# Kernel tuning notes

Hardware: AMD Instinct MI355X
Metric: run time of the kernel (lower is better)

The kernel has to match this reference:

```python
import jax, jax.numpy as jnp
import numpy as np

NX, NY, NZ = 432, 496, 1
C = 64
B = 4
P = 64000


def setup_inputs() -> dict:
    key = jax.random.key(0)
    k1, k2, k3 = jax.random.split(key, 3)
    pillar_features = jax.random.normal(k1, (P, C), dtype=jnp.float32)
    # Build unique (batch, y, x) cells so the scatter has no duplicate targets
    # (torch advanced-index assignment with duplicates is order-dependent).
    n_cells = B * NY * NX
    flat = jax.random.permutation(k2, n_cells)[:P]  # unique global cell ids
    b = flat // (NY * NX)
    rem = flat % (NY * NX)
    y = rem // NX
    x = rem % NX
    z = jnp.zeros_like(b)
    voxel_coords = jnp.stack([b, z, y, x], axis=1).astype(jnp.int32)  # [P, 4]
    return {
        "pillar_features": pillar_features,
        "voxel_coords": voxel_coords,
        "batch_size": B,
    }


def reference(pillar_features, voxel_coords, batch_size):
    # Global scatter: one fused pass instead of the per-batch Python loop.
    coords = voxel_coords.astype(jnp.int32)
    # per-sample spatial index, exactly as in the torch code: z + y*nx + x
    spatial_idx = coords[:, 1] + coords[:, 2] * NX + coords[:, 3]
    global_idx = coords[:, 0] * (NY * NX) + spatial_idx  # [P]
    canvas = jnp.zeros((batch_size * NZ * NY * NX, pillar_features.shape[1]),
                       dtype=pillar_features.dtype)
    canvas = canvas.at[global_idx].set(pillar_features)  # [B*ny*nx, C]
    # -> [B, C, ny, nx], matching view(batch, C*nz, ny, nx)
    spatial = canvas.reshape(batch_size, NY, NX, -1).transpose(0, 3, 1, 2)
    return spatial
```

## Files before the change

### kernel.cpp

```cpp
#include <hip/hip_runtime.h>

#define PNX 432
#define PNY 496
#define PNC 64
#define PLANE (PNY * PNX)


__global__ void pp_init_map(int4* __restrict__ map4, int n4) {
    int t = blockIdx.x * blockDim.x + threadIdx.x;
    if (t < n4) {
        map4[t] = make_int4(-1, -1, -1, -1);
    }
}

__global__ void pp_scatter_map(const int4* __restrict__ coords,
                               int* __restrict__ map, int P) {
    int p = blockIdx.x * blockDim.x + threadIdx.x;
    if (p >= P) return;
    int4 c = coords[p];
    int gidx = c.x * PLANE + c.y + c.z * PNX + c.w;
    map[gidx] = p;
}

__global__ void pp_gather(const float* __restrict__ feat,
                          const int* __restrict__ map,
                          float* __restrict__ out, int ncells4) {
    int t = blockIdx.x * blockDim.x + threadIdx.x;
    if (t >= ncells4) return;
    int cell0 = t * 4;
    int b = cell0 / PLANE;
    int spat = cell0 - b * PLANE;

    int4 pm = *reinterpret_cast<const int4*>(map + cell0);
    const float* f0 = feat + (long)pm.x * PNC;
    const float* f1 = feat + (long)pm.y * PNC;
    const float* f2 = feat + (long)pm.z * PNC;
    const float* f3 = feat + (long)pm.w * PNC;

    float4* outbase =
        reinterpret_cast<float4*>(out + (size_t)b * PNC * PLANE + spat);

    #pragma unroll 8
    for (int c = 0; c < PNC; ++c) {
        float4 v;
        v.x = (pm.x >= 0) ? f0[c] : 0.0f;
        v.y = (pm.y >= 0) ? f1[c] : 0.0f;
        v.z = (pm.z >= 0) ? f2[c] : 0.0f;
        v.w = (pm.w >= 0) ? f3[c] : 0.0f;
        outbase[(size_t)c * (PLANE / 4)] = v;
    }
}


__global__ void pp_zero_out(float4* __restrict__ out4, size_t n4) {
    size_t t = (size_t)blockIdx.x * blockDim.x + threadIdx.x;
    size_t stride = (size_t)gridDim.x * blockDim.x;
    float4 z = make_float4(0.f, 0.f, 0.f, 0.f);
    for (size_t i = t; i < n4; i += stride) out4[i] = z;
}

__global__ void pp_scatter_direct(const float* __restrict__ feat,
                                  const int4* __restrict__ coords,
                                  float* __restrict__ out, int P) {
    int t = blockIdx.x * blockDim.x + threadIdx.x;
    int p = t >> 6;
    int c = t & 63;
    if (p >= P) return;
    int4 co = coords[p];
    size_t oidx = ((size_t)(co.x * PNC + c)) * PLANE + co.y + co.z * PNX + co.w;
    out[oidx] = feat[p * PNC + c];
}

extern "C" void kernel_launch(void* const* d_in, const int* in_sizes, int n_in,
                              void* d_out, int out_size, void* d_ws, size_t ws_size,
                              hipStream_t stream) {
    const float* feat = (const float*)d_in[0];
    const int4* coords = (const int4*)d_in[1];
    float* out = (float*)d_out;

    const int P = in_sizes[0] / PNC;
    const int B = out_size / (PNC * PLANE);
    const int ncells = B * PLANE;
    const size_t mapBytes = (size_t)ncells * sizeof(int);

    if (ws_size >= mapBytes) {
        int* map = (int*)d_ws;
        int n4 = ncells / 4;
        pp_init_map<<<(n4 + 255) / 256, 256, 0, stream>>>((int4*)map, n4);
        pp_scatter_map<<<(P + 255) / 256, 256, 0, stream>>>(coords, map, P);
        pp_gather<<<(n4 + 255) / 256, 256, 0, stream>>>(feat, map, out, n4);
    } else {
        size_t n4 = (size_t)out_size / 4;
        pp_zero_out<<<2048, 256, 0, stream>>>((float4*)out, n4);
        int total = P * PNC;
        pp_scatter_direct<<<(total + 255) / 256, 256, 0, stream>>>(feat, coords, out, P);
    }
}
```

Before: 50.55 us.

## Split gather over channel groups with vector loads and nontemporal stores

The gather kernel now uses a 2D grid, where each blockIdx.y handles 16 channels. Each thread loads float4 chunks of feature rows, transposes them in registers and writes them with nontemporal 16-byte stores. The map-init kernel is replaced with hipMemsetAsync. The aim is to cut scalar loads, increase parallelism and avoid cache pollution on the large output write, at the cost of reading the map four times.

```diff
diff --git a/kernel.cpp b/kernel.cpp
--- a/kernel.cpp
+++ b/kernel.cpp
@@ -5,13 +5,8 @@
 #define PNC 64
 #define PLANE (PNY * PNX)
 
+typedef float f32x4 __attribute__((ext_vector_type(4)));
 
-__global__ void pp_init_map(int4* __restrict__ map4, int n4) {
-    int t = blockIdx.x * blockDim.x + threadIdx.x;
-    if (t < n4) {
-        map4[t] = make_int4(-1, -1, -1, -1);
-    }
-}
 
 __global__ void pp_scatter_map(const int4* __restrict__ coords,
                                int* __restrict__ map, int P) {
@@ -24,38 +19,46 @@
 
 __global__ void pp_gather(const float* __restrict__ feat,
                           const int* __restrict__ map,
-                          float* __restrict__ out, int ncells4) {
+                          float* __restrict__ out, int n4) {
     int t = blockIdx.x * blockDim.x + threadIdx.x;
-    if (t >= ncells4) return;
+    if (t >= n4) return;
     int cell0 = t * 4;
     int b = cell0 / PLANE;
     int spat = cell0 - b * PLANE;
+    int cbase = blockIdx.y * (PNC / 4);
 
     int4 pm = *reinterpret_cast<const int4*>(map + cell0);
-    const float* f0 = feat + (long)pm.x * PNC;
-    const float* f1 = feat + (long)pm.y * PNC;
-    const float* f2 = feat + (long)pm.z * PNC;
-    const float* f3 = feat + (long)pm.w * PNC;
+    const f32x4* fp0 = reinterpret_cast<const f32x4*>(feat + (long)pm.x * PNC + cbase);
+    const f32x4* fp1 = reinterpret_cast<const f32x4*>(feat + (long)pm.y * PNC + cbase);
+    const f32x4* fp2 = reinterpret_cast<const f32x4*>(feat + (long)pm.z * PNC + cbase);
+    const f32x4* fp3 = reinterpret_cast<const f32x4*>(feat + (long)pm.w * PNC + cbase);
 
-    float4* outbase =
-        reinterpret_cast<float4*>(out + (size_t)b * PNC * PLANE + spat);
+    float* outp = out + (size_t)b * PNC * PLANE + (size_t)cbase * PLANE + spat;
+    const f32x4 z = {0.f, 0.f, 0.f, 0.f};
 
-    #pragma unroll 8
-    for (int c = 0; c < PNC; ++c) {
-        float4 v;
-        v.x = (pm.x >= 0) ? f0[c] : 0.0f;
-        v.y = (pm.y >= 0) ? f1[c] : 0.0f;
-        v.z = (pm.z >= 0) ? f2[c] : 0.0f;
-        v.w = (pm.w >= 0) ? f3[c] : 0.0f;
-        outbase[(size_t)c * (PLANE / 4)] = v;
+    #pragma unroll
+    for (int g = 0; g < 4; ++g) {
+        f32x4 r0 = (pm.x >= 0) ? fp0[g] : z;
+        f32x4 r1 = (pm.y >= 0) ? fp1[g] : z;
+        f32x4 r2 = (pm.z >= 0) ? fp2[g] : z;
+        f32x4 r3 = (pm.w >= 0) ? fp3[g] : z;
+        f32x4 o0 = {r0.x, r1.x, r2.x, r3.x};
+        f32x4 o1 = {r0.y, r1.y, r2.y, r3.y};
+        f32x4 o2 = {r0.z, r1.z, r2.z, r3.z};
+        f32x4 o3 = {r0.w, r1.w, r2.w, r3.w};
+        float* o = outp + (size_t)(g * 4) * PLANE;
+        __builtin_nontemporal_store(o0, reinterpret_cast<f32x4*>(o));
+        __builtin_nontemporal_store(o1, reinterpret_cast<f32x4*>(o + PLANE));
+        __builtin_nontemporal_store(o2, reinterpret_cast<f32x4*>(o + 2 * PLANE));
+        __builtin_nontemporal_store(o3, reinterpret_cast<f32x4*>(o + 3 * PLANE));
     }
 }
 
 
-__global__ void pp_zero_out(float4* __restrict__ out4, size_t n4) {
+__global__ void pp_zero_out(f32x4* __restrict__ out4, size_t n4) {
     size_t t = (size_t)blockIdx.x * blockDim.x + threadIdx.x;
     size_t stride = (size_t)gridDim.x * blockDim.x;
-    float4 z = make_float4(0.f, 0.f, 0.f, 0.f);
+    const f32x4 z = {0.f, 0.f, 0.f, 0.f};
     for (size_t i = t; i < n4; i += stride) out4[i] = z;
 }
 
@@ -86,12 +89,13 @@
     if (ws_size >= mapBytes) {
         int* map = (int*)d_ws;
         int n4 = ncells / 4;
-        pp_init_map<<<(n4 + 255) / 256, 256, 0, stream>>>((int4*)map, n4);
+        (void)hipMemsetAsync(map, 0xFF, mapBytes, stream);
         pp_scatter_map<<<(P + 255) / 256, 256, 0, stream>>>(coords, map, P);
-        pp_gather<<<(n4 + 255) / 256, 256, 0, stream>>>(feat, map, out, n4);
+        dim3 grid((n4 + 255) / 256, 4);
+        pp_gather<<<grid, 256, 0, stream>>>(feat, map, out, n4);
     } else {
         size_t n4 = (size_t)out_size / 4;
-        pp_zero_out<<<2048, 256, 0, stream>>>((float4*)out, n4);
+        pp_zero_out<<<2048, 256, 0, stream>>>((f32x4*)out, n4);
         int total = P * PNC;
         pp_scatter_direct<<<(total + 255) / 256, 256, 0, stream>>>(feat, coords, out, P);
     }
```

Result: slower. 55.34 us (+9.5%).
